# Performance work log

Hardware: AMD Instinct MI355X
Metric: run time of the kernel (lower is better)

## Reference

```python
import jax, jax.numpy as jnp
import numpy as np

B, H, W, C = 16, 64, 64, 256


def setup_inputs() -> dict:
    key = jax.random.key(0)
    k1, k2, k3 = jax.random.split(key, 3)
    x = jax.random.normal(k1, (B, H, W, C), dtype=jnp.float32)
    # 1x1 convs are channel matmuls; lecun_normal ~ N(0, 1/fan_in)
    W_qkv = jax.random.normal(k2, (C, 3 * C), dtype=jnp.float32) / np.sqrt(C)
    W_out = jax.random.normal(k3, (C, C), dtype=jnp.float32) / np.sqrt(C)
    b_out = jnp.zeros((C,), dtype=jnp.float32)
    return {"x": x, "W_qkv": W_qkv, "W_out": W_out, "b_out": b_out}


def reference(x, W_qkv, W_out, b_out):
    b, h, w, c = x.shape
    n = h * w
    # to_qkv: 1x1 conv, no bias -> channel matmul
    qkv = jnp.einsum('bhwc,cd->bhwd', x, W_qkv)            # [b,h,w,3c]
    q, k, v = jnp.split(qkv, 3, axis=-1)                    # each [b,h,w,c]
    # rearrange to [b, c, n] (heads=1)
    q = q.reshape(b, n, c).transpose(0, 2, 1)
    k = k.reshape(b, n, c).transpose(0, 2, 1)
    v = v.reshape(b, n, c).transpose(0, 2, 1)
    k = jax.nn.softmax(k, axis=-1)                          # softmax over spatial n
    context = jnp.einsum('bdn,ben->bde', k, v)              # [b,c,c] per-sample context
    out = jnp.einsum('bde,bdn->ben', context, q)            # [b,c,n]
    out = out.reshape(b, c, h, w).transpose(0, 2, 3, 1)     # [b,h,w,c]
    # to_out: 1x1 conv with bias
    return jnp.einsum('bhwc,cd->bhwd', out, W_out) + b_out
```

## Files before the change

kernel.cpp:

```cpp
#include <hip/hip_runtime.h>
#include <hip/hip_bf16.h>


typedef __bf16 bf16;
typedef __bf16 bf16x4 __attribute__((ext_vector_type(4)));
typedef __bf16 bf16x8 __attribute__((ext_vector_type(8)));
typedef float  f32x4  __attribute__((ext_vector_type(4)));

#define LDP 72

__device__ __forceinline__ bf16 tob(float f) { return (bf16)f; }

__device__ __forceinline__ void gl_lds16(const void* g, void* l) {
  __builtin_amdgcn_global_load_lds(
      (const __attribute__((address_space(1))) void*)g,
      (__attribute__((address_space(3))) void*)l, 16, 0, 0);
}

__device__ __forceinline__ void stage_swz(const bf16* __restrict__ src,
                                          size_t stride, bf16* lds, int tid) {
#pragma unroll
  for (int r = 0; r < 4; ++r) {
    int si = r * 256 + tid;
    int row = si >> 3, c16 = si & 7;
    int gcol = (c16 ^ (row & 7)) << 3;
    gl_lds16(src + (size_t)row * stride + gcol, lds + si * 8);
  }
}

__device__ __forceinline__ void compute_tile_swz(const bf16* As, const bf16* Bs,
                                                 f32x4 acc[4][4], int wr, int wc,
                                                 int lr, int g) {
#pragma unroll
  for (int ks = 0; ks < 2; ++ks) {
    int slot = ((ks * 4 + g) ^ (lr & 7)) * 8;
    bf16x8 a[4], b[4];
#pragma unroll
    for (int m = 0; m < 4; ++m)
      a[m] = *reinterpret_cast<const bf16x8*>(&As[(wr * 64 + m * 16 + lr) * 64 + slot]);
#pragma unroll
    for (int n = 0; n < 4; ++n)
      b[n] = *reinterpret_cast<const bf16x8*>(&Bs[(wc * 64 + n * 16 + lr) * 64 + slot]);
#pragma unroll
    for (int m = 0; m < 4; ++m)
#pragma unroll
      for (int n = 0; n < 4; ++n)
        acc[m][n] = __builtin_amdgcn_mfma_f32_16x16x32_bf16(a[m], b[n], acc[m][n], 0, 0, 0);
  }
}

__device__ __forceinline__ void compute_tileP2(const bf16* As, const bf16* Bs,
                                               f32x4 acc[4][2], int wr, int wc,
                                               int lr, int g) {
#pragma unroll
  for (int ks = 0; ks < 2; ++ks) {
    bf16x8 a[4], b[2];
#pragma unroll
    for (int m = 0; m < 4; ++m)
      a[m] = *reinterpret_cast<const bf16x8*>(&As[(wr * 64 + m * 16 + lr) * LDP + ks * 32 + g * 8]);
#pragma unroll
    for (int n = 0; n < 2; ++n)
      b[n] = *reinterpret_cast<const bf16x8*>(&Bs[(wc * 32 + n * 16 + lr) * LDP + ks * 32 + g * 8]);
#pragma unroll
    for (int m = 0; m < 4; ++m)
#pragma unroll
      for (int n = 0; n < 2; ++n)
        acc[m][n] = __builtin_amdgcn_mfma_f32_16x16x32_bf16(a[m], b[n], acc[m][n], 0, 0, 0);
  }
}

__global__ __launch_bounds__(256) void k_prep(const float* __restrict__ x,
                                              const float* __restrict__ Wq,
                                              const float* __restrict__ Wo,
                                              bf16* __restrict__ xb,
                                              bf16* __restrict__ WqT,
                                              bf16* __restrict__ WoT,
                                              float* __restrict__ S) {
  int b = blockIdx.x, tid = threadIdx.x;
  if (b < 4096) {
    size_t base = (size_t)b * 4096;
#pragma unroll
    for (int r = 0; r < 4; ++r) {
      size_t e = base + r * 1024 + tid * 4;
      float4 v = *reinterpret_cast<const float4*>(x + e);
      bf16x4 p;
      p[0] = tob(v.x); p[1] = tob(v.y); p[2] = tob(v.z); p[3] = tob(v.w);
      *reinterpret_cast<bf16x4*>(xb + e) = p;
    }
    if (b < 16) S[b * 256 + tid] = 0.0f;
  } else {
    int i0 = (b - 4096) * 1024 + tid * 4;
#pragma unroll
    for (int j = 0; j < 4; ++j) {
      int idx = i0 + j;
      if (idx < 196608) {
        int n = idx >> 8, k = idx & 255;
        WqT[idx] = tob(Wq[(size_t)k * 768 + n]);
      } else {
        int i2 = idx - 196608;
        int co = i2 >> 8, e2 = i2 & 255;
        WoT[i2] = tob(Wo[(size_t)e2 * 256 + co]);
      }
    }
  }
}

__global__ __launch_bounds__(256) void k_qkv(const bf16* __restrict__ xb,
                                             const bf16* __restrict__ WqT,
                                             bf16* __restrict__ Q,
                                             bf16* __restrict__ Et,
                                             bf16* __restrict__ Vt,
                                             float* __restrict__ S) {
  __shared__ __align__(16) bf16 As0[8192], Bs0[8192], As1[8192], Bs1[8192];
  int bx = blockIdx.x;
  int swz = (bx & 7) * 384 + (bx >> 3);
  int rb = swz / 6, cb = swz % 6;
  int tid = threadIdx.x;
  int lane = tid & 63, w = tid >> 6;
  int wr = w >> 1, wc = w & 1;
  int g = lane >> 4, lr = lane & 15;
  const int rowbase = rb * 128, colbase = cb * 128;
  const bf16* Ab = xb + (size_t)rowbase * 256;
  const bf16* Bb = WqT + (size_t)colbase * 256;

  f32x4 acc[4][4];
#pragma unroll
  for (int m = 0; m < 4; ++m)
#pragma unroll
    for (int n = 0; n < 4; ++n) acc[m][n] = (f32x4)0.0f;

  stage_swz(Ab, 256, As0, tid);
  stage_swz(Bb, 256, Bs0, tid);
  __syncthreads();
#pragma unroll
  for (int kp = 0; kp < 2; ++kp) {
    int kt = kp * 2;
    stage_swz(Ab + (kt + 1) * 64, 256, As1, tid);
    stage_swz(Bb + (kt + 1) * 64, 256, Bs1, tid);
    compute_tile_swz(As0, Bs0, acc, wr, wc, lr, g);
    __syncthreads();
    if (kt + 2 < 4) {
      stage_swz(Ab + (kt + 2) * 64, 256, As0, tid);
      stage_swz(Bb + (kt + 2) * 64, 256, Bs0, tid);
    }
    compute_tile_swz(As1, Bs1, acc, wr, wc, lr, g);
    if (kt + 2 < 4) __syncthreads();
  }

  int grow = rowbase + wr * 64;
  int gcol = colbase + wc * 64;
  int sec = gcol >> 8;
  int coff = gcol & 255;
  int b = grow >> 12;
  int nsp = grow & 4095;

  if (sec == 0) {
#pragma unroll
    for (int m = 0; m < 4; ++m)
#pragma unroll
      for (int n = 0; n < 4; ++n) {
        int col = coff + n * 16 + lr;
#pragma unroll
        for (int t = 0; t < 4; ++t) {
          int row = grow + m * 16 + g * 4 + t;
          Q[(size_t)row * 256 + col] = tob(acc[m][n][t]);
        }
      }
  } else {
    bf16* dst = (sec == 1) ? Et : Vt;
    float cs0 = 0.f, cs1 = 0.f, cs2 = 0.f, cs3 = 0.f;
#pragma unroll
    for (int m = 0; m < 4; ++m)
#pragma unroll
      for (int n = 0; n < 4; ++n) {
        int col = coff + n * 16 + lr;
        int nn0 = nsp + m * 16 + g * 4;
        bf16x4 p;
#pragma unroll
        for (int t = 0; t < 4; ++t) {
          float v = acc[m][n][t];
          if (sec == 1) {
            v = expf(v);
            if (n == 0) cs0 += v; else if (n == 1) cs1 += v;
            else if (n == 2) cs2 += v; else cs3 += v;
          }
          p[t] = tob(v);
        }
        *reinterpret_cast<bf16x4*>(&dst[((size_t)(b * 256 + col) << 12) + nn0]) = p;
      }
    if (sec == 1) {
      cs0 += __shfl_xor(cs0, 16); cs0 += __shfl_xor(cs0, 32);
      cs1 += __shfl_xor(cs1, 16); cs1 += __shfl_xor(cs1, 32);
      cs2 += __shfl_xor(cs2, 16); cs2 += __shfl_xor(cs2, 32);
      cs3 += __shfl_xor(cs3, 16); cs3 += __shfl_xor(cs3, 32);
      float v = (g == 0) ? cs0 : (g == 1) ? cs1 : (g == 2) ? cs2 : cs3;
      atomicAdd(&S[b * 256 + coff + g * 16 + lr], v);
    }
  }
}

__global__ __launch_bounds__(256) void k_ctx(const bf16* __restrict__ Et,
                                             const bf16* __restrict__ Vt,
                                             bf16* __restrict__ part) {
  __shared__ __align__(16) bf16 As0[8192], Bs0[8192], As1[8192], Bs1[8192];
  int bx = blockIdx.x;
  int swz = (bx & 7) * 64 + (bx >> 3);
  int tile = swz & 3, dblk = tile >> 1, eblk = tile & 1;
  int s = (swz >> 2) & 7;
  int b = swz >> 5;
  int tid = threadIdx.x;
  int lane = tid & 63, w = tid >> 6;
  int wr = w >> 1, wc = w & 1;
  int g = lane >> 4, lr = lane & 15;

  const bf16* Ab = Et + (((size_t)(b * 256 + dblk * 128)) << 12) + s * 512;
  const bf16* Bb = Vt + (((size_t)(b * 256 + eblk * 128)) << 12) + s * 512;

  f32x4 acc[4][4];
#pragma unroll
  for (int m = 0; m < 4; ++m)
#pragma unroll
    for (int n = 0; n < 4; ++n) acc[m][n] = (f32x4)0.0f;

  stage_swz(Ab, 4096, As0, tid);
  stage_swz(Bb, 4096, Bs0, tid);
  __syncthreads();
#pragma unroll
  for (int kp = 0; kp < 4; ++kp) {
    int kt = kp * 2;
    stage_swz(Ab + (kt + 1) * 64, 4096, As1, tid);
    stage_swz(Bb + (kt + 1) * 64, 4096, Bs1, tid);
    compute_tile_swz(As0, Bs0, acc, wr, wc, lr, g);
    __syncthreads();
    if (kt + 2 < 8) {
      stage_swz(Ab + (kt + 2) * 64, 4096, As0, tid);
      stage_swz(Bb + (kt + 2) * 64, 4096, Bs0, tid);
    }
    compute_tile_swz(As1, Bs1, acc, wr, wc, lr, g);
    if (kt + 2 < 8) __syncthreads();
  }

  bf16* p = part + (size_t)(b * 8 + s) * 65536;
  int dbase = dblk * 128 + wr * 64;
  int ebase = eblk * 128 + wc * 64;
#pragma unroll
  for (int m = 0; m < 4; ++m)
#pragma unroll
    for (int n = 0; n < 4; ++n)
#pragma unroll
      for (int t = 0; t < 4; ++t)
        p[(size_t)(dbase + m * 16 + g * 4 + t) * 256 + ebase + n * 16 + lr] = tob(acc[m][n][t]);
}

__global__ __launch_bounds__(256) void k_wc(const bf16* __restrict__ part,
                                            const float* __restrict__ S,
                                            const bf16* __restrict__ WoT,
                                            bf16* __restrict__ WcT) {
  __shared__ __align__(16) bf16 As[128 * LDP];
  __shared__ __align__(16) bf16 Bs[64 * LDP];
  int bx = blockIdx.x;
  int b = bx >> 3, dblk = (bx >> 2) & 1, cblk = bx & 3;
  int tid = threadIdx.x;
  int lane = tid & 63, w = tid >> 6;
  int wr = w >> 1, wc = w & 1;
  int g = lane >> 4, lr = lane & 15;
  const bf16* p0 = part + (size_t)b * 8 * 65536;

  f32x4 acc[4][2];
#pragma unroll
  for (int m = 0; m < 4; ++m)
#pragma unroll
    for (int n = 0; n < 2; ++n) acc[m][n] = (f32x4)0.0f;

  for (int kt = 0; kt < 4; ++kt) {
    int k0 = kt * 64;
    __syncthreads();
#pragma unroll
    for (int r = 0; r < 8; ++r) {
      int idx = r * 1024 + tid * 4;
      int row = idx >> 6, col = idx & 63;
      int d = dblk * 128 + row;
      size_t off = (size_t)d * 256 + k0 + col;
      float s0 = 0.f, s1 = 0.f, s2 = 0.f, s3 = 0.f;
#pragma unroll
      for (int sl = 0; sl < 8; ++sl) {
        bf16x4 v = *reinterpret_cast<const bf16x4*>(p0 + (size_t)sl * 65536 + off);
        s0 += (float)v[0]; s1 += (float)v[1]; s2 += (float)v[2]; s3 += (float)v[3];
      }
      float rs = 1.0f / S[b * 256 + d];
      bf16x4 p;
      p[0] = tob(s0 * rs); p[1] = tob(s1 * rs); p[2] = tob(s2 * rs); p[3] = tob(s3 * rs);
      *reinterpret_cast<bf16x4*>(&As[row * LDP + col]) = p;
    }
#pragma unroll
    for (int r = 0; r < 2; ++r) {
      int idx = r * 2048 + tid * 8;
      int row = idx >> 6, col = idx & 63;
      bf16x8 v = *reinterpret_cast<const bf16x8*>(WoT + (size_t)(cblk * 64 + row) * 256 + k0 + col);
      *reinterpret_cast<bf16x8*>(&Bs[row * LDP + col]) = v;
    }
    __syncthreads();
    compute_tileP2(As, Bs, acc, wr, wc, lr, g);
  }

  int dbase = dblk * 128 + wr * 64;
  int cbase = cblk * 64 + wc * 32;
#pragma unroll
  for (int m = 0; m < 4; ++m)
#pragma unroll
    for (int n = 0; n < 2; ++n) {
      int co = cbase + n * 16 + lr;
      int d0 = dbase + m * 16 + g * 4;
      bf16x4 p;
#pragma unroll
      for (int t = 0; t < 4; ++t) p[t] = tob(acc[m][n][t]);
      *reinterpret_cast<bf16x4*>(&WcT[(size_t)b * 65536 + (size_t)co * 256 + d0]) = p;
    }
}

__global__ __launch_bounds__(256) void k_out(const bf16* __restrict__ Q,
                                             const bf16* __restrict__ WcT,
                                             const float* __restrict__ b_out,
                                             float* __restrict__ y) {
  __shared__ __align__(16) bf16 As0[8192], Bs0[8192], As1[8192], Bs1[8192];
  int bx = blockIdx.x;
  int swz = (bx & 7) * 128 + (bx >> 3);
  int rb = swz >> 1, cbk = swz & 1;
  int tid = threadIdx.x;
  int lane = tid & 63, w = tid >> 6;
  int wr = w >> 1, wc = w & 1;
  int g = lane >> 4, lr = lane & 15;
  int rowbase = rb * 128;
  int b = rowbase >> 12;
  const bf16* Ab = Q + (size_t)rowbase * 256;
  const bf16* Bb = WcT + (size_t)b * 65536 + (size_t)(cbk * 128) * 256;

  f32x4 acc[4][4];
#pragma unroll
  for (int m = 0; m < 4; ++m)
#pragma unroll
    for (int n = 0; n < 4; ++n) acc[m][n] = (f32x4)0.0f;

  stage_swz(Ab, 256, As0, tid);
  stage_swz(Bb, 256, Bs0, tid);
  __syncthreads();
#pragma unroll
  for (int kp = 0; kp < 2; ++kp) {
    int kt = kp * 2;
    stage_swz(Ab + (kt + 1) * 64, 256, As1, tid);
    stage_swz(Bb + (kt + 1) * 64, 256, Bs1, tid);
    compute_tile_swz(As0, Bs0, acc, wr, wc, lr, g);
    __syncthreads();
    if (kt + 2 < 4) {
      stage_swz(Ab + (kt + 2) * 64, 256, As0, tid);
      stage_swz(Bb + (kt + 2) * 64, 256, Bs0, tid);
    }
    compute_tile_swz(As1, Bs1, acc, wr, wc, lr, g);
    if (kt + 2 < 4) __syncthreads();
  }

  int cbase = cbk * 128 + wc * 64;
#pragma unroll
  for (int m = 0; m < 4; ++m)
#pragma unroll
    for (int n = 0; n < 4; ++n) {
      int col = cbase + n * 16 + lr;
      float bo = b_out[col];
#pragma unroll
      for (int t = 0; t < 4; ++t) {
        int row = rowbase + wr * 64 + m * 16 + g * 4 + t;
        y[(size_t)row * 256 + col] = acc[m][n][t] + bo;
      }
    }
}

extern "C" void kernel_launch(void* const* d_in, const int* in_sizes, int n_in,
                              void* d_out, int out_size, void* d_ws, size_t ws_size,
                              hipStream_t stream) {
  (void)in_sizes; (void)n_in; (void)out_size; (void)ws_size;
  const float* x  = (const float*)d_in[0];
  const float* Wq = (const float*)d_in[1];
  const float* Wo = (const float*)d_in[2];
  const float* bo = (const float*)d_in[3];
  float* y = (float*)d_out;

  char* ws = (char*)d_ws;
  bf16*  Q    = (bf16*)(ws);
  bf16*  Et   = (bf16*)(ws + 33554432);
  bf16*  Vt   = (bf16*)(ws + 67108864);
  bf16*  xb   = (bf16*)(ws + 100663296);
  bf16*  part = (bf16*)(ws + 100663296);
  bf16*  WcT  = (bf16*)(ws + 134217728);
  bf16*  WqT  = (bf16*)(ws + 136314880);
  bf16*  WoT  = (bf16*)(ws + 136708096);
  float* S    = (float*)(ws + 136839168);

  k_prep<<<dim3(4352), dim3(256), 0, stream>>>(x, Wq, Wo, xb, WqT, WoT, S);
  k_qkv<<<dim3(3072), dim3(256), 0, stream>>>(xb, WqT, Q, Et, Vt, S);
  k_ctx<<<dim3(512), dim3(256), 0, stream>>>(Et, Vt, part);
  k_wc<<<dim3(128), dim3(256), 0, stream>>>(part, S, WoT, WcT);
  k_out<<<dim3(1024), dim3(256), 0, stream>>>(Q, WcT, bo, y);
}
```

Baseline: 228.1 us.

## Fuse fp32-to-bf16 cast of x into QKV GEMM and halve ctx split-K

```diff
diff --git a/kernel.cpp b/kernel.cpp
--- a/kernel.cpp
+++ b/kernel.cpp
@@ -28,6 +28,30 @@
   }
 }
 
+__device__ __forceinline__ void loadA_f32(const float* __restrict__ src,
+                                          int tid, float4 va[4], float4 vb[4]) {
+#pragma unroll
+  for (int r = 0; r < 4; ++r) {
+    int si = r * 256 + tid;
+    int row = si >> 3, c16 = si & 7;
+    int gcol = (c16 ^ (row & 7)) << 3;
+    const float* s = src + (size_t)row * 256 + gcol;
+    va[r] = *reinterpret_cast<const float4*>(s);
+    vb[r] = *reinterpret_cast<const float4*>(s + 4);
+  }
+}
+__device__ __forceinline__ void writeA(bf16* lds, int tid,
+                                       const float4 va[4], const float4 vb[4]) {
+#pragma unroll
+  for (int r = 0; r < 4; ++r) {
+    int si = r * 256 + tid;
+    bf16x8 p;
+    p[0] = tob(va[r].x); p[1] = tob(va[r].y); p[2] = tob(va[r].z); p[3] = tob(va[r].w);
+    p[4] = tob(vb[r].x); p[5] = tob(vb[r].y); p[6] = tob(vb[r].z); p[7] = tob(vb[r].w);
+    *reinterpret_cast<bf16x8*>(&lds[si * 8]) = p;
+  }
+}
+
 __device__ __forceinline__ void compute_tile_swz(const bf16* As, const bf16* Bs,
                                                  f32x4 acc[4][4], int wr, int wc,
                                                  int lr, int g) {
@@ -69,43 +93,28 @@
   }
 }
 
-__global__ __launch_bounds__(256) void k_prep(const float* __restrict__ x,
-                                              const float* __restrict__ Wq,
+__global__ __launch_bounds__(256) void k_prep(const float* __restrict__ Wq,
                                               const float* __restrict__ Wo,
-                                              bf16* __restrict__ xb,
                                               bf16* __restrict__ WqT,
                                               bf16* __restrict__ WoT,
                                               float* __restrict__ S) {
-  int b = blockIdx.x, tid = threadIdx.x;
-  if (b < 4096) {
-    size_t base = (size_t)b * 4096;
-#pragma unroll
-    for (int r = 0; r < 4; ++r) {
-      size_t e = base + r * 1024 + tid * 4;
-      float4 v = *reinterpret_cast<const float4*>(x + e);
-      bf16x4 p;
-      p[0] = tob(v.x); p[1] = tob(v.y); p[2] = tob(v.z); p[3] = tob(v.w);
-      *reinterpret_cast<bf16x4*>(xb + e) = p;
-    }
-    if (b < 16) S[b * 256 + tid] = 0.0f;
-  } else {
-    int i0 = (b - 4096) * 1024 + tid * 4;
-#pragma unroll
-    for (int j = 0; j < 4; ++j) {
-      int idx = i0 + j;
-      if (idx < 196608) {
-        int n = idx >> 8, k = idx & 255;
-        WqT[idx] = tob(Wq[(size_t)k * 768 + n]);
-      } else {
-        int i2 = idx - 196608;
-        int co = i2 >> 8, e2 = i2 & 255;
-        WoT[i2] = tob(Wo[(size_t)e2 * 256 + co]);
-      }
-    }
-  }
-}
-
-__global__ __launch_bounds__(256) void k_qkv(const bf16* __restrict__ xb,
+  int i0 = blockIdx.x * 1024 + threadIdx.x * 4;
+#pragma unroll
+  for (int j = 0; j < 4; ++j) {
+    int idx = i0 + j;
+    if (idx < 196608) {
+      int n = idx >> 8, k = idx & 255;
+      WqT[idx] = tob(Wq[(size_t)k * 768 + n]);
+    } else {
+      int i2 = idx - 196608;
+      int co = i2 >> 8, e2 = i2 & 255;
+      WoT[i2] = tob(Wo[(size_t)e2 * 256 + co]);
+    }
+    if (idx < 4096) S[idx] = 0.0f;
+  }
+}
+
+__global__ __launch_bounds__(256) void k_qkv(const float* __restrict__ x,
                                              const bf16* __restrict__ WqT,
                                              bf16* __restrict__ Q,
                                              bf16* __restrict__ Et,
@@ -120,7 +129,7 @@
   int wr = w >> 1, wc = w & 1;
   int g = lane >> 4, lr = lane & 15;
   const int rowbase = rb * 128, colbase = cb * 128;
-  const bf16* Ab = xb + (size_t)rowbase * 256;
+  const float* Ax = x + (size_t)rowbase * 256;
   const bf16* Bb = WqT + (size_t)colbase * 256;
 
   f32x4 acc[4][4];
@@ -129,22 +138,26 @@
 #pragma unroll
     for (int n = 0; n < 4; ++n) acc[m][n] = (f32x4)0.0f;
 
-  stage_swz(Ab, 256, As0, tid);
+  float4 va[4], vb[4];
+  loadA_f32(Ax, tid, va, vb);
   stage_swz(Bb, 256, Bs0, tid);
+  writeA(As0, tid, va, vb);
   __syncthreads();
 #pragma unroll
-  for (int kp = 0; kp < 2; ++kp) {
-    int kt = kp * 2;
-    stage_swz(Ab + (kt + 1) * 64, 256, As1, tid);
-    stage_swz(Bb + (kt + 1) * 64, 256, Bs1, tid);
-    compute_tile_swz(As0, Bs0, acc, wr, wc, lr, g);
-    __syncthreads();
-    if (kt + 2 < 4) {
-      stage_swz(Ab + (kt + 2) * 64, 256, As0, tid);
-      stage_swz(Bb + (kt + 2) * 64, 256, Bs0, tid);
-    }
-    compute_tile_swz(As1, Bs1, acc, wr, wc, lr, g);
-    if (kt + 2 < 4) __syncthreads();
+  for (int kt = 0; kt < 4; ++kt) {
+    bf16* Ac = (kt & 1) ? As1 : As0;
+    bf16* Bc = (kt & 1) ? Bs1 : Bs0;
+    bf16* An = (kt & 1) ? As0 : As1;
+    bf16* Bn = (kt & 1) ? Bs0 : Bs1;
+    if (kt < 3) {
+      loadA_f32(Ax + (kt + 1) * 64, tid, va, vb);
+      stage_swz(Bb + (kt + 1) * 64, 256, Bn, tid);
+    }
+    compute_tile_swz(Ac, Bc, acc, wr, wc, lr, g);
+    if (kt < 3) {
+      writeA(An, tid, va, vb);
+      __syncthreads();
+    }
   }
 
   int grow = rowbase + wr * 64;
@@ -204,17 +217,17 @@
                                              bf16* __restrict__ part) {
   __shared__ __align__(16) bf16 As0[8192], Bs0[8192], As1[8192], Bs1[8192];
   int bx = blockIdx.x;
-  int swz = (bx & 7) * 64 + (bx >> 3);
-  int tile = swz & 3, dblk = tile >> 1, eblk = tile & 1;
-  int s = (swz >> 2) & 7;
-  int b = swz >> 5;
+  int swz = (bx & 7) * 32 + (bx >> 3);
+  int s = swz & 3;
+  int quad = (swz >> 2) & 3, dblk = quad >> 1, eblk = quad & 1;
+  int b = swz >> 4;
   int tid = threadIdx.x;
   int lane = tid & 63, w = tid >> 6;
   int wr = w >> 1, wc = w & 1;
   int g = lane >> 4, lr = lane & 15;
 
-  const bf16* Ab = Et + (((size_t)(b * 256 + dblk * 128)) << 12) + s * 512;
-  const bf16* Bb = Vt + (((size_t)(b * 256 + eblk * 128)) << 12) + s * 512;
+  const bf16* Ab = Et + (((size_t)(b * 256 + dblk * 128)) << 12) + s * 1024;
+  const bf16* Bb = Vt + (((size_t)(b * 256 + eblk * 128)) << 12) + s * 1024;
 
   f32x4 acc[4][4];
 #pragma unroll
@@ -226,21 +239,21 @@
   stage_swz(Bb, 4096, Bs0, tid);
   __syncthreads();
 #pragma unroll
-  for (int kp = 0; kp < 4; ++kp) {
+  for (int kp = 0; kp < 8; ++kp) {
     int kt = kp * 2;
     stage_swz(Ab + (kt + 1) * 64, 4096, As1, tid);
     stage_swz(Bb + (kt + 1) * 64, 4096, Bs1, tid);
     compute_tile_swz(As0, Bs0, acc, wr, wc, lr, g);
     __syncthreads();
-    if (kt + 2 < 8) {
+    if (kt + 2 < 16) {
       stage_swz(Ab + (kt + 2) * 64, 4096, As0, tid);
       stage_swz(Bb + (kt + 2) * 64, 4096, Bs0, tid);
     }
     compute_tile_swz(As1, Bs1, acc, wr, wc, lr, g);
-    if (kt + 2 < 8) __syncthreads();
-  }
-
-  bf16* p = part + (size_t)(b * 8 + s) * 65536;
+    if (kt + 2 < 16) __syncthreads();
+  }
+
+  bf16* p = part + (size_t)(b * 4 + s) * 65536;
   int dbase = dblk * 128 + wr * 64;
   int ebase = eblk * 128 + wc * 64;
 #pragma unroll
@@ -264,7 +277,7 @@
   int lane = tid & 63, w = tid >> 6;
   int wr = w >> 1, wc = w & 1;
   int g = lane >> 4, lr = lane & 15;
-  const bf16* p0 = part + (size_t)b * 8 * 65536;
+  const bf16* p0 = part + (size_t)b * 4 * 65536;
 
   f32x4 acc[4][2];
 #pragma unroll
@@ -283,7 +296,7 @@
       size_t off = (size_t)d * 256 + k0 + col;
       float s0 = 0.f, s1 = 0.f, s2 = 0.f, s3 = 0.f;
 #pragma unroll
-      for (int sl = 0; sl < 8; ++sl) {
+      for (int sl = 0; sl < 4; ++sl) {
         bf16x4 v = *reinterpret_cast<const bf16x4*>(p0 + (size_t)sl * 65536 + off);
         s0 += (float)v[0]; s1 += (float)v[1]; s2 += (float)v[2]; s3 += (float)v[3];
       }
@@ -388,16 +401,15 @@
   bf16*  Q    = (bf16*)(ws);
   bf16*  Et   = (bf16*)(ws + 33554432);
   bf16*  Vt   = (bf16*)(ws + 67108864);
-  bf16*  xb   = (bf16*)(ws + 100663296);
   bf16*  part = (bf16*)(ws + 100663296);
   bf16*  WcT  = (bf16*)(ws + 134217728);
   bf16*  WqT  = (bf16*)(ws + 136314880);
   bf16*  WoT  = (bf16*)(ws + 136708096);
   float* S    = (float*)(ws + 136839168);
 
-  k_prep<<<dim3(4352), dim3(256), 0, stream>>>(x, Wq, Wo, xb, WqT, WoT, S);
-  k_qkv<<<dim3(3072), dim3(256), 0, stream>>>(xb, WqT, Q, Et, Vt, S);
-  k_ctx<<<dim3(512), dim3(256), 0, stream>>>(Et, Vt, part);
+  k_prep<<<dim3(256), dim3(256), 0, stream>>>(Wq, Wo, WqT, WoT, S);
+  k_qkv<<<dim3(3072), dim3(256), 0, stream>>>(x, WqT, Q, Et, Vt, S);
+  k_ctx<<<dim3(256), dim3(256), 0, stream>>>(Et, Vt, part);
   k_wc<<<dim3(128), dim3(256), 0, stream>>>(part, S, WoT, WcT);
   k_out<<<dim3(1024), dim3(256), 0, stream>>>(Q, WcT, bo, y);
 }
```

Result: slower. 240.5 us (+5.4%).
